# Kernel tuning notes

Hardware: AMD Instinct MI355X
Metric: run time of the kernel (lower is better)

## Reference

```python
import jax, jax.numpy as jnp
import numpy as np


def _gcn(x, src, dst, W, b, n):
    # symmetric normalization: deg computed on edges WITH self-loops (weights 1)
    deg = jax.ops.segment_sum(jnp.ones_like(src, dtype=x.dtype), dst, num_segments=n)
    dinv = jnp.where(deg > 0, jax.lax.rsqrt(deg), 0.0)
    norm = dinv[src] * dinv[dst]              # [E+n]
    xw = x @ W                                # [n, out] transform first (cheaper)
    msg = xw[src] * norm[:, None]             # gather + edge scale
    return jax.ops.segment_sum(msg, dst, num_segments=n) + b


def setup_inputs() -> dict:
    key = jax.random.key(0)
    ks = jax.random.split(key, 8)
    N, E = 100_000, 1_280_000
    x = jax.random.normal(ks[0], (N, 18), dtype=jnp.float32)
    edge_index = jax.random.randint(ks[1], (2, E), 0, N, dtype=jnp.int32)
    W1 = jax.random.normal(ks[2], (18, 32), dtype=jnp.float32) * 0.2
    b1 = jnp.zeros((32,), dtype=jnp.float32)
    W2 = jax.random.normal(ks[3], (32, 64), dtype=jnp.float32) * 0.15
    b2 = jnp.zeros((64,), dtype=jnp.float32)
    Wfc = jax.random.normal(ks[4], (64, 2), dtype=jnp.float32) * 0.1
    bfc = jnp.zeros((2,), dtype=jnp.float32)
    return {"x": x, "edge_index": edge_index, "W1": W1, "b1": b1,
            "W2": W2, "b2": b2, "Wfc": Wfc, "bfc": bfc}


def reference(x, edge_index, W1, b1, W2, b2, Wfc, bfc):
    n = x.shape[0]
    loop = jnp.arange(n, dtype=edge_index.dtype)
    src = jnp.concatenate([edge_index[0], loop])   # add self-loops (PyG default)
    dst = jnp.concatenate([edge_index[1], loop])
    h = jax.nn.relu(_gcn(x, src, dst, W1, b1, n))
    h = jax.nn.relu(_gcn(h, src, dst, W2, b2, n))
    logits = h @ Wfc + bfc
    return jax.nn.log_softmax(logits, axis=1)
```

## Files before the change

kernel.cpp:

```cpp
#include <hip/hip_runtime.h>
#include <math.h>


#define TPB 256
#define BSH 8
#define BNODES 256
#define MAXBUCK 512
#define CH 4096
#define CAPSH 13
#define CAP (1 << CAPSH)

__global__ void k_part(const int* __restrict__ src, const int* __restrict__ dst,
                       int* __restrict__ bcursor, int* __restrict__ eb,
                       float* __restrict__ u1f, float* __restrict__ u2f,
                       int E, int n, int nbuck) {
    __shared__ int lh[MAXBUCK];
    __shared__ int lbase[MAXBUCK];
    int t = threadIdx.x;
    if (blockIdx.x == 0 && t < 32) {
        u1f[(size_t)n * 32 + t] = 0.f;
        u2f[(size_t)n * 32 + t] = 0.f;
    }
    int chunk0 = blockIdx.x * CH;
    int end = min(chunk0 + CH, E);
    const int4* dst4 = (const int4*)dst;
    const int4* src4 = (const int4*)src;
    for (int i = t; i < nbuck; i += TPB) lh[i] = 0;
    __syncthreads();
    for (int e4 = chunk0 / 4 + t; e4 * 4 < end; e4 += TPB) {
        int base = e4 * 4;
        int4 d = dst4[e4];
        if (base + 0 < end) atomicAdd(&lh[d.x >> BSH], 1);
        if (base + 1 < end) atomicAdd(&lh[d.y >> BSH], 1);
        if (base + 2 < end) atomicAdd(&lh[d.z >> BSH], 1);
        if (base + 3 < end) atomicAdd(&lh[d.w >> BSH], 1);
    }
    __syncthreads();
    for (int i = t; i < nbuck; i += TPB) {
        int c = lh[i];
        lbase[i] = c ? atomicAdd(&bcursor[i], c) : 0;
        lh[i] = 0;
    }
    __syncthreads();
    for (int e4 = chunk0 / 4 + t; e4 * 4 < end; e4 += TPB) {
        int base = e4 * 4;
        int4 d = dst4[e4];
        int4 s = src4[e4];
        #define PUT(c, sv) if (base + c < end) { \
            int b = (d.sv) >> BSH; \
            int r = lbase[b] + atomicAdd(&lh[b], 1); \
            if (r < CAP) \
                eb[((size_t)b << CAPSH) + r] = ((s.sv) << BSH) | ((d.sv) & (BNODES - 1)); }
        PUT(0, x) PUT(1, y) PUT(2, z) PUT(3, w)
        #undef PUT
    }
}

__global__ void k_bucket(const int* __restrict__ eb, const int* __restrict__ bcursor,
                         const float* __restrict__ x,
                         int* __restrict__ csr, int* __restrict__ row_start,
                         int* __restrict__ cnt4, float* __restrict__ dinv,
                         float* __restrict__ u1f, int n) {
    __shared__ int lcnt[BNODES];
    __shared__ int lscan[BNODES];
    __shared__ float ldinv[BNODES];
    int b = blockIdx.x;
    int t = threadIdx.x;
    int node0 = b << BSH;
    int beg = b << CAPSH;
    int end = beg + min(bcursor[b], CAP);
    lcnt[t] = 0;
    __syncthreads();
    for (int i = beg + t; i < end; i += TPB)
        atomicAdd(&lcnt[eb[i] & (BNODES - 1)], 1);
    __syncthreads();
    int v = lcnt[t];
    int pad = (v + 3) & ~3;
    lscan[t] = pad;
    __syncthreads();
    for (int off = 1; off < TPB; off <<= 1) {
        int xx = (t >= off) ? lscan[t - off] : 0;
        __syncthreads();
        lscan[t] += xx;
        __syncthreads();
    }
    int pexcl = lscan[t] - pad;
    int node = node0 + t;
    float dv = rsqrtf(1.0f + (float)v);
    ldinv[t] = dv;
    if (node < n) {
        row_start[node] = beg + pexcl;
        cnt4[node] = pad >> 2;
        dinv[node] = dv;
    }
    __syncthreads();
    lcnt[t] = pexcl;
    __syncthreads();
    for (int i = beg + t; i < end; i += TPB) {
        int e = eb[i];
        int p = atomicAdd(&lcnt[e & (BNODES - 1)], 1);
        csr[beg + p] = e >> BSH;
    }
    __syncthreads();
    for (int p = v; p < pad; ++p) csr[beg + pexcl + p] = n;
    int nn = min(BNODES, n - node0);
    int tot = nn * 32;
    const float* xb = x + (size_t)node0 * 18;
    float* ub = u1f + (size_t)node0 * 32;
    for (int i = t; i < tot; i += TPB) {
        int nl = i >> 5, f = i & 31;
        ub[i] = (f < 18) ? xb[nl * 18 + f] * ldinv[nl] : 0.f;
    }
}

__global__ void k_fused1(const float4* __restrict__ u1q, const int* __restrict__ row_start,
                         const int* __restrict__ cnt4, const int* __restrict__ csr,
                         const float* __restrict__ dinv, const float* __restrict__ W1,
                         const float* __restrict__ b1, float* __restrict__ u2f,
                         int n) {
    __shared__ float lagg[4][8][40];
    int t = threadIdx.x;
    int lane = t & 63, wv = t >> 6;
    int q = lane & 7, grp = lane >> 3;
    int f = lane & 31, h = lane >> 5;
    float w1r[18];
#pragma unroll
    for (int k = 0; k < 18; ++k) w1r[k] = W1[k * 32 + f];
    float b1v = b1[f];
    int node0 = (blockIdx.x * 4 + wv) * 8;
    int node = node0 + grp;
    float4 acc = make_float4(0.f, 0.f, 0.f, 0.f);
    if (node < n) {
        acc = u1q[(size_t)node * 8 + q];
        int beg = row_start[node];
        int it = cnt4[node];
        const int4* ip = (const int4*)(csr + beg);
        for (int i = 0; i < it; ++i) {
            int4 s = ip[i];
            float4 v0 = u1q[(size_t)s.x * 8 + q];
            float4 v1 = u1q[(size_t)s.y * 8 + q];
            float4 v2 = u1q[(size_t)s.z * 8 + q];
            float4 v3 = u1q[(size_t)s.w * 8 + q];
            acc.x += (v0.x + v1.x) + (v2.x + v3.x);
            acc.y += (v0.y + v1.y) + (v2.y + v3.y);
            acc.z += (v0.z + v1.z) + (v2.z + v3.z);
            acc.w += (v0.w + v1.w) + (v2.w + v3.w);
        }
    }
    *(float4*)&lagg[wv][grp][4 * q] = acc;
#pragma unroll
    for (int r = 0; r < 4; ++r) {
        int nl = 2 * r + h;
        int nodeT = node0 + nl;
        if (nodeT < n) {
            const float* rp = lagg[wv][nl];
            float a = 0.f;
#pragma unroll
            for (int k = 0; k < 18; ++k) a = fmaf(rp[k], w1r[k], a);
            float di = dinv[nodeT];
            u2f[(size_t)nodeT * 32 + f] = fmaxf(fmaf(di, a, b1v), 0.f) * di;
        }
    }
}

__global__ void k_fused2(const float4* __restrict__ u2q, const int* __restrict__ row_start,
                         const int* __restrict__ cnt4, const int* __restrict__ csr,
                         const float* __restrict__ dinv, const float* __restrict__ W2,
                         const float* __restrict__ b2, const float* __restrict__ Wfc,
                         const float* __restrict__ bfc, float* __restrict__ out,
                         int n) {
    __shared__ float lagg[4][8][40];
    int t = threadIdx.x;
    int lane = t & 63, wv = t >> 6;
    int q = lane & 7, grp = lane >> 3;
    float w2r[32];
#pragma unroll
    for (int k = 0; k < 32; ++k) w2r[k] = W2[k * 64 + lane];
    float b2v = b2[lane];
    float wf0 = Wfc[lane * 2 + 0], wf1 = Wfc[lane * 2 + 1];
    float bf0 = bfc[0], bf1 = bfc[1];
    int node0 = (blockIdx.x * 4 + wv) * 8;
    int node = node0 + grp;
    float4 acc = make_float4(0.f, 0.f, 0.f, 0.f);
    if (node < n) {
        acc = u2q[(size_t)node * 8 + q];
        int beg = row_start[node];
        int it = cnt4[node];
        const int4* ip = (const int4*)(csr + beg);
        for (int i = 0; i < it; ++i) {
            int4 s = ip[i];
            float4 v0 = u2q[(size_t)s.x * 8 + q];
            float4 v1 = u2q[(size_t)s.y * 8 + q];
            float4 v2 = u2q[(size_t)s.z * 8 + q];
            float4 v3 = u2q[(size_t)s.w * 8 + q];
            acc.x += (v0.x + v1.x) + (v2.x + v3.x);
            acc.y += (v0.y + v1.y) + (v2.y + v3.y);
            acc.z += (v0.z + v1.z) + (v2.z + v3.z);
            acc.w += (v0.w + v1.w) + (v2.w + v3.w);
        }
    }
    *(float4*)&lagg[wv][grp][4 * q] = acc;
#pragma unroll
    for (int r = 0; r < 8; ++r) {
        int nodeT = node0 + r;
        const float* rp = lagg[wv][r];
        float c0 = 0.f, c1 = 0.f, c2 = 0.f, c3 = 0.f;
#pragma unroll
        for (int k = 0; k < 32; k += 4) {
            c0 = fmaf(rp[k],     w2r[k],     c0);
            c1 = fmaf(rp[k + 1], w2r[k + 1], c1);
            c2 = fmaf(rp[k + 2], w2r[k + 2], c2);
            c3 = fmaf(rp[k + 3], w2r[k + 3], c3);
        }
        float a = (c0 + c1) + (c2 + c3);
        float v = (nodeT < n) ? fmaxf(fmaf(dinv[nodeT], a, b2v), 0.f) : 0.f;
        float l0 = v * wf0;
        float l1 = v * wf1;
#pragma unroll
        for (int off = 32; off >= 1; off >>= 1) {
            l0 += __shfl_xor(l0, off, 64);
            l1 += __shfl_xor(l1, off, 64);
        }
        if (lane == 0 && nodeT < n) {
            l0 += bf0;
            l1 += bf1;
            float m2 = fmaxf(l0, l1);
            float lse = m2 + logf(expf(l0 - m2) + expf(l1 - m2));
            out[nodeT * 2 + 0] = l0 - lse;
            out[nodeT * 2 + 1] = l1 - lse;
        }
    }
}

extern "C" void kernel_launch(void* const* d_in, const int* in_sizes, int n_in,
                              void* d_out, int out_size, void* d_ws, size_t ws_size,
                              hipStream_t stream) {
    const float* x   = (const float*)d_in[0];
    const int*   ei  = (const int*)d_in[1];
    const float* W1  = (const float*)d_in[2];
    const float* b1  = (const float*)d_in[3];
    const float* W2  = (const float*)d_in[4];
    const float* b2  = (const float*)d_in[5];
    const float* Wfc = (const float*)d_in[6];
    const float* bfc = (const float*)d_in[7];
    float* out = (float*)d_out;

    const int n = in_sizes[0] / 18;
    const int E = in_sizes[1] / 2;
    const int* src = ei;
    const int* dst = ei + E;
    const int nbuck = (n + BNODES - 1) >> BSH;

    char* w = (char*)d_ws;
    int*    bcursor   = (int*)w;     w += (size_t)nbuck * 4;
    int*    row_start = (int*)w;     w += (size_t)n * 4;
    int*    cnt4      = (int*)w;     w += (size_t)n * 4;
    float*  dinv      = (float*)w;   w += (size_t)n * 4;
    int*    eb        = (int*)w;     w += (size_t)nbuck * CAP * 4;
    int*    csr       = (int*)w;     w += (size_t)nbuck * CAP * 4;
    w = (char*)(((size_t)w + 127) & ~(size_t)127);
    float*  u1f       = (float*)w;   w += (size_t)(n + 1) * 32 * 4;
    w = (char*)(((size_t)w + 127) & ~(size_t)127);
    float*  u2f       = (float*)w;   w += (size_t)(n + 1) * 32 * 4;

    hipMemsetAsync(bcursor, 0, (size_t)nbuck * 4, stream);
    k_part<<<(E + CH - 1) / CH, TPB, 0, stream>>>(src, dst, bcursor, eb, u1f, u2f, E, n, nbuck);
    k_bucket<<<nbuck, TPB, 0, stream>>>(eb, bcursor, x, csr, row_start, cnt4, dinv, u1f, n);

    const int waves = (n + 7) / 8;
    const int blocksF = (waves + 3) / 4;

    k_fused1<<<blocksF, TPB, 0, stream>>>((const float4*)u1f, row_start, cnt4, csr,
                                          dinv, W1, b1, u2f, n);
    k_fused2<<<blocksF, TPB, 0, stream>>>((const float4*)u2f, row_start, cnt4, csr,
                                          dinv, W2, b2, Wfc, bfc, out, n);
}
```

Baseline: 180.8 us.

## Aggregate directly from destination buckets with shared-memory atomics, dropping CSR build

Removes the per-bucket CSR construction (prefix scan, scatter, padding) and instead has each 1024-thread block own one 256-node bucket. The block accumulates neighbor features into shared memory with float atomics while streaming the unsorted bucket edge list, then applies the dense transform. This saves a full CSR write/read pass and the padding sentinel row. In exchange it adds LDS atomic contention and runs only ~391 large blocks, about one per CU, which may limit latency hiding for the random gathers.

Result: slower. 701.7 us (+288.2%).

```diff
diff --git a/kernel.cpp b/kernel.cpp
--- a/kernel.cpp
+++ b/kernel.cpp
@@ -3,24 +3,21 @@
 
 
 #define TPB 256
+#define LTPB 1024
 #define BSH 8
 #define BNODES 256
 #define MAXBUCK 512
 #define CH 4096
 #define CAPSH 13
 #define CAP (1 << CAPSH)
+#define LSTR 36
 
 __global__ void k_part(const int* __restrict__ src, const int* __restrict__ dst,
                        int* __restrict__ bcursor, int* __restrict__ eb,
-                       float* __restrict__ u1f, float* __restrict__ u2f,
-                       int E, int n, int nbuck) {
+                       int E, int nbuck) {
     __shared__ int lh[MAXBUCK];
     __shared__ int lbase[MAXBUCK];
     int t = threadIdx.x;
-    if (blockIdx.x == 0 && t < 32) {
-        u1f[(size_t)n * 32 + t] = 0.f;
-        u2f[(size_t)n * 32 + t] = 0.f;
-    }
     int chunk0 = blockIdx.x * CH;
     int end = min(chunk0 + CH, E);
     const int4* dst4 = (const int4*)dst;
@@ -56,13 +53,10 @@
     }
 }
 
-__global__ void k_bucket(const int* __restrict__ eb, const int* __restrict__ bcursor,
-                         const float* __restrict__ x,
-                         int* __restrict__ csr, int* __restrict__ row_start,
-                         int* __restrict__ cnt4, float* __restrict__ dinv,
-                         float* __restrict__ u1f, int n) {
+__global__ void k_prep(const int* __restrict__ eb, const int* __restrict__ bcursor,
+                       const float* __restrict__ x, float* __restrict__ dinv,
+                       float* __restrict__ u1f, int n) {
     __shared__ int lcnt[BNODES];
-    __shared__ int lscan[BNODES];
     __shared__ float ldinv[BNODES];
     int b = blockIdx.x;
     int t = threadIdx.x;
@@ -74,35 +68,11 @@
     for (int i = beg + t; i < end; i += TPB)
         atomicAdd(&lcnt[eb[i] & (BNODES - 1)], 1);
     __syncthreads();
-    int v = lcnt[t];
-    int pad = (v + 3) & ~3;
-    lscan[t] = pad;
-    __syncthreads();
-    for (int off = 1; off < TPB; off <<= 1) {
-        int xx = (t >= off) ? lscan[t - off] : 0;
-        __syncthreads();
-        lscan[t] += xx;
-        __syncthreads();
-    }
-    int pexcl = lscan[t] - pad;
     int node = node0 + t;
-    float dv = rsqrtf(1.0f + (float)v);
+    float dv = rsqrtf(1.0f + (float)lcnt[t]);
     ldinv[t] = dv;
-    if (node < n) {
-        row_start[node] = beg + pexcl;
-        cnt4[node] = pad >> 2;
-        dinv[node] = dv;
-    }
-    __syncthreads();
-    lcnt[t] = pexcl;
-    __syncthreads();
-    for (int i = beg + t; i < end; i += TPB) {
-        int e = eb[i];
-        int p = atomicAdd(&lcnt[e & (BNODES - 1)], 1);
-        csr[beg + p] = e >> BSH;
-    }
-    __syncthreads();
-    for (int p = v; p < pad; ++p) csr[beg + pexcl + p] = n;
+    if (node < n) dinv[node] = dv;
+    __syncthreads();
     int nn = min(BNODES, n - node0);
     int tot = nn * 32;
     const float* xb = x + (size_t)node0 * 18;
@@ -113,107 +83,110 @@
     }
 }
 
-__global__ void k_fused1(const float4* __restrict__ u1q, const int* __restrict__ row_start,
-                         const int* __restrict__ cnt4, const int* __restrict__ csr,
-                         const float* __restrict__ dinv, const float* __restrict__ W1,
-                         const float* __restrict__ b1, float* __restrict__ u2f,
-                         int n) {
-    __shared__ float lagg[4][8][40];
+__global__ void __launch_bounds__(LTPB, 1)
+k_layer1(const float4* __restrict__ u1q, const int* __restrict__ eb,
+         const int* __restrict__ bcursor, const float* __restrict__ dinv,
+         const float* __restrict__ W1, const float* __restrict__ b1,
+         float* __restrict__ u2f, int n) {
+    __shared__ float lagg[BNODES][LSTR];
+    int b = blockIdx.x;
     int t = threadIdx.x;
     int lane = t & 63, wv = t >> 6;
-    int q = lane & 7, grp = lane >> 3;
-    int f = lane & 31, h = lane >> 5;
+    int q = lane & 7, g = lane >> 3;
+    int h = lane >> 5, f = lane & 31;
+    int node0 = b << BSH;
+    for (int i = t; i < BNODES * 32; i += LTPB) {
+        int nl = i >> 5, ff = i & 31;
+        int node = node0 + nl;
+        lagg[nl][ff] = (node < n) ? ((const float*)u1q)[(size_t)node * 32 + ff] : 0.f;
+    }
     float w1r[18];
 #pragma unroll
     for (int k = 0; k < 18; ++k) w1r[k] = W1[k * 32 + f];
     float b1v = b1[f];
-    int node0 = (blockIdx.x * 4 + wv) * 8;
-    int node = node0 + grp;
-    float4 acc = make_float4(0.f, 0.f, 0.f, 0.f);
-    if (node < n) {
-        acc = u1q[(size_t)node * 8 + q];
-        int beg = row_start[node];
-        int it = cnt4[node];
-        const int4* ip = (const int4*)(csr + beg);
-        for (int i = 0; i < it; ++i) {
-            int4 s = ip[i];
-            float4 v0 = u1q[(size_t)s.x * 8 + q];
-            float4 v1 = u1q[(size_t)s.y * 8 + q];
-            float4 v2 = u1q[(size_t)s.z * 8 + q];
-            float4 v3 = u1q[(size_t)s.w * 8 + q];
-            acc.x += (v0.x + v1.x) + (v2.x + v3.x);
-            acc.y += (v0.y + v1.y) + (v2.y + v3.y);
-            acc.z += (v0.z + v1.z) + (v2.z + v3.z);
-            acc.w += (v0.w + v1.w) + (v2.w + v3.w);
-        }
-    }
-    *(float4*)&lagg[wv][grp][4 * q] = acc;
-#pragma unroll
-    for (int r = 0; r < 4; ++r) {
-        int nl = 2 * r + h;
-        int nodeT = node0 + nl;
-        if (nodeT < n) {
-            const float* rp = lagg[wv][nl];
+    __syncthreads();
+    int nE = min(bcursor[b], CAP);
+    const int* ebb = eb + ((size_t)b << CAPSH);
+    for (int base = wv * 8; base < nE; base += 16 * 8) {
+        int e = base + g;
+        if (e < nE) {
+            int pk = ebb[e];
+            int s = pk >> BSH, d = pk & (BNODES - 1);
+            float4 v = u1q[(size_t)s * 8 + q];
+            atomicAdd(&lagg[d][4 * q + 0], v.x);
+            atomicAdd(&lagg[d][4 * q + 1], v.y);
+            atomicAdd(&lagg[d][4 * q + 2], v.z);
+            atomicAdd(&lagg[d][4 * q + 3], v.w);
+        }
+    }
+    __syncthreads();
+#pragma unroll
+    for (int r = 0; r < 8; ++r) {
+        int nl = r * 32 + wv * 2 + h;
+        int node = node0 + nl;
+        if (node < n) {
             float a = 0.f;
 #pragma unroll
-            for (int k = 0; k < 18; ++k) a = fmaf(rp[k], w1r[k], a);
-            float di = dinv[nodeT];
-            u2f[(size_t)nodeT * 32 + f] = fmaxf(fmaf(di, a, b1v), 0.f) * di;
-        }
-    }
-}
-
-__global__ void k_fused2(const float4* __restrict__ u2q, const int* __restrict__ row_start,
-                         const int* __restrict__ cnt4, const int* __restrict__ csr,
-                         const float* __restrict__ dinv, const float* __restrict__ W2,
-                         const float* __restrict__ b2, const float* __restrict__ Wfc,
-                         const float* __restrict__ bfc, float* __restrict__ out,
-                         int n) {
-    __shared__ float lagg[4][8][40];
+            for (int k = 0; k < 18; ++k) a = fmaf(lagg[nl][k], w1r[k], a);
+            float di = dinv[node];
+            u2f[(size_t)node * 32 + f] = fmaxf(fmaf(di, a, b1v), 0.f) * di;
+        }
+    }
+}
+
+__global__ void __launch_bounds__(LTPB, 1)
+k_layer2(const float4* __restrict__ u2q, const int* __restrict__ eb,
+         const int* __restrict__ bcursor, const float* __restrict__ dinv,
+         const float* __restrict__ W2, const float* __restrict__ b2,
+         const float* __restrict__ Wfc, const float* __restrict__ bfc,
+         float* __restrict__ out, int n) {
+    __shared__ float lagg[BNODES][LSTR];
+    int b = blockIdx.x;
     int t = threadIdx.x;
     int lane = t & 63, wv = t >> 6;
-    int q = lane & 7, grp = lane >> 3;
+    int q = lane & 7, g = lane >> 3;
+    int node0 = b << BSH;
+    for (int i = t; i < BNODES * 32; i += LTPB) {
+        int nl = i >> 5, ff = i & 31;
+        int node = node0 + nl;
+        lagg[nl][ff] = (node < n) ? ((const float*)u2q)[(size_t)node * 32 + ff] : 0.f;
+    }
     float w2r[32];
 #pragma unroll
     for (int k = 0; k < 32; ++k) w2r[k] = W2[k * 64 + lane];
     float b2v = b2[lane];
     float wf0 = Wfc[lane * 2 + 0], wf1 = Wfc[lane * 2 + 1];
     float bf0 = bfc[0], bf1 = bfc[1];
-    int node0 = (blockIdx.x * 4 + wv) * 8;
-    int node = node0 + grp;
-    float4 acc = make_float4(0.f, 0.f, 0.f, 0.f);
-    if (node < n) {
-        acc = u2q[(size_t)node * 8 + q];
-        int beg = row_start[node];
-        int it = cnt4[node];
-        const int4* ip = (const int4*)(csr + beg);
-        for (int i = 0; i < it; ++i) {
-            int4 s = ip[i];
-            float4 v0 = u2q[(size_t)s.x * 8 + q];
-            float4 v1 = u2q[(size_t)s.y * 8 + q];
-            float4 v2 = u2q[(size_t)s.z * 8 + q];
-            float4 v3 = u2q[(size_t)s.w * 8 + q];
-            acc.x += (v0.x + v1.x) + (v2.x + v3.x);
-            acc.y += (v0.y + v1.y) + (v2.y + v3.y);
-            acc.z += (v0.z + v1.z) + (v2.z + v3.z);
-            acc.w += (v0.w + v1.w) + (v2.w + v3.w);
-        }
-    }
-    *(float4*)&lagg[wv][grp][4 * q] = acc;
-#pragma unroll
-    for (int r = 0; r < 8; ++r) {
-        int nodeT = node0 + r;
-        const float* rp = lagg[wv][r];
+    __syncthreads();
+    int nE = min(bcursor[b], CAP);
+    const int* ebb = eb + ((size_t)b << CAPSH);
+    for (int base = wv * 8; base < nE; base += 16 * 8) {
+        int e = base + g;
+        if (e < nE) {
+            int pk = ebb[e];
+            int s = pk >> BSH, d = pk & (BNODES - 1);
+            float4 v = u2q[(size_t)s * 8 + q];
+            atomicAdd(&lagg[d][4 * q + 0], v.x);
+            atomicAdd(&lagg[d][4 * q + 1], v.y);
+            atomicAdd(&lagg[d][4 * q + 2], v.z);
+            atomicAdd(&lagg[d][4 * q + 3], v.w);
+        }
+    }
+    __syncthreads();
+#pragma unroll 4
+    for (int r = 0; r < 16; ++r) {
+        int nl = r * 16 + wv;
+        int node = node0 + nl;
         float c0 = 0.f, c1 = 0.f, c2 = 0.f, c3 = 0.f;
 #pragma unroll
         for (int k = 0; k < 32; k += 4) {
-            c0 = fmaf(rp[k],     w2r[k],     c0);
-            c1 = fmaf(rp[k + 1], w2r[k + 1], c1);
-            c2 = fmaf(rp[k + 2], w2r[k + 2], c2);
-            c3 = fmaf(rp[k + 3], w2r[k + 3], c3);
+            c0 = fmaf(lagg[nl][k],     w2r[k],     c0);
+            c1 = fmaf(lagg[nl][k + 1], w2r[k + 1], c1);
+            c2 = fmaf(lagg[nl][k + 2], w2r[k + 2], c2);
+            c3 = fmaf(lagg[nl][k + 3], w2r[k + 3], c3);
         }
         float a = (c0 + c1) + (c2 + c3);
-        float v = (nodeT < n) ? fmaxf(fmaf(dinv[nodeT], a, b2v), 0.f) : 0.f;
+        float v = (node < n) ? fmaxf(fmaf(dinv[node], a, b2v), 0.f) : 0.f;
         float l0 = v * wf0;
         float l1 = v * wf1;
 #pragma unroll
@@ -221,13 +194,13 @@
             l0 += __shfl_xor(l0, off, 64);
             l1 += __shfl_xor(l1, off, 64);
         }
-        if (lane == 0 && nodeT < n) {
+        if (lane == 0 && node < n) {
             l0 += bf0;
             l1 += bf1;
             float m2 = fmaxf(l0, l1);
             float lse = m2 + logf(expf(l0 - m2) + expf(l1 - m2));
-            out[nodeT * 2 + 0] = l0 - lse;
-            out[nodeT * 2 + 1] = l1 - lse;
+            out[node * 2 + 0] = l0 - lse;
+            out[node * 2 + 1] = l1 - lse;
         }
     }
 }
@@ -252,26 +225,20 @@
     const int nbuck = (n + BNODES - 1) >> BSH;
 
     char* w = (char*)d_ws;
-    int*    bcursor   = (int*)w;     w += (size_t)nbuck * 4;
-    int*    row_start = (int*)w;     w += (size_t)n * 4;
-    int*    cnt4      = (int*)w;     w += (size_t)n * 4;
-    float*  dinv      = (float*)w;   w += (size_t)n * 4;
-    int*    eb        = (int*)w;     w += (size_t)nbuck * CAP * 4;
-    int*    csr       = (int*)w;     w += (size_t)nbuck * CAP * 4;
+    int*    bcursor = (int*)w;     w += (size_t)nbuck * 4;
+    float*  dinv    = (float*)w;   w += (size_t)n * 4;
+    int*    eb      = (int*)w;     w += (size_t)nbuck * CAP * 4;
     w = (char*)(((size_t)w + 127) & ~(size_t)127);
-    float*  u1f       = (float*)w;   w += (size_t)(n + 1) * 32 * 4;
+    float*  u1f     = (float*)w;   w += (size_t)n * 32 * 4;
     w = (char*)(((size_t)w + 127) & ~(size_t)127);
-    float*  u2f       = (float*)w;   w += (size_t)(n + 1) * 32 * 4;
+    float*  u2f     = (float*)w;   w += (size_t)n * 32 * 4;
 
     hipMemsetAsync(bcursor, 0, (size_t)nbuck * 4, stream);
-    k_part<<<(E + CH - 1) / CH, TPB, 0, stream>>>(src, dst, bcursor, eb, u1f, u2f, E, n, nbuck);
-    k_bucket<<<nbuck, TPB, 0, stream>>>(eb, bcursor, x, csr, row_start, cnt4, dinv, u1f, n);
-
-    const int waves = (n + 7) / 8;
-    const int blocksF = (waves + 3) / 4;
-
-    k_fused1<<<blocksF, TPB, 0, stream>>>((const float4*)u1f, row_start, cnt4, csr,
-                                          dinv, W1, b1, u2f, n);
-    k_fused2<<<blocksF, TPB, 0, stream>>>((const float4*)u2f, row_start, cnt4, csr,
-                                          dinv, W2, b2, Wfc, bfc, out, n);
-}
+    k_part<<<(E + CH - 1) / CH, TPB, 0, stream>>>(src, dst, bcursor, eb, E, nbuck);
+    k_prep<<<nbuck, TPB, 0, stream>>>(eb, bcursor, x, dinv, u1f, n);
+
+    k_layer1<<<nbuck, LTPB, 0, stream>>>((const float4*)u1f, eb, bcursor, dinv,
+                                         W1, b1, u2f, n);
+    k_layer2<<<nbuck, LTPB, 0, stream>>>((const float4*)u2f, eb, bcursor, dinv,
+                                         W2, b2, Wfc, bfc, out, n);
+}
```
